# Kernel optimization log

Measured on AMD Instinct MI355X. Metric: run time of the kernel, lower is better.

## Reference

```python
import jax, jax.numpy as jnp
import numpy as np

D = 1024
H = 16
DH = D // H
F = 4096
EPS = 1e-5

def layernorm(x, gamma, beta):
    mean = jnp.mean(x, axis=-1, keepdims=True)
    var = jnp.mean((x - mean) ** 2, axis=-1, keepdims=True)  # biased variance
    return gamma * (x - mean) / jnp.sqrt(var + EPS) + beta

def setup_inputs() -> dict:
    key = jax.random.key(0)
    ks = jax.random.split(key, 12)
    s = 1.0 / np.sqrt(D)
    sf = 1.0 / np.sqrt(F)
    return {
        "x": jax.random.normal(ks[0], (16, 512, D), dtype=jnp.float32),
        "Wq": jax.random.normal(ks[1], (H, D, DH), dtype=jnp.float32) * s,
        "Wk": jax.random.normal(ks[2], (H, D, DH), dtype=jnp.float32) * s,
        "Wv": jax.random.normal(ks[3], (H, D, DH), dtype=jnp.float32) * s,
        "Wo": jax.random.normal(ks[4], (D, D), dtype=jnp.float32) * s,
        "bo": jax.random.normal(ks[5], (D,), dtype=jnp.float32) * s,
        "gamma1": jnp.ones((D,), dtype=jnp.float32),
        "beta1": jnp.zeros((D,), dtype=jnp.float32),
        "gamma2": jnp.ones((D,), dtype=jnp.float32),
        "beta2": jnp.zeros((D,), dtype=jnp.float32),
        "W1": jax.random.normal(ks[6], (D, F), dtype=jnp.float32) * s,
        "b1": jax.random.normal(ks[7], (F,), dtype=jnp.float32) * s,
        "W2": jax.random.normal(ks[8], (F, D), dtype=jnp.float32) * sf,
        "b2": jax.random.normal(ks[9], (D,), dtype=jnp.float32) * sf,
    }

def reference(x, Wq, Wk, Wv, Wo, bo, gamma1, beta1, gamma2, beta2, W1, b1, W2, b2):
    B, S, _ = x.shape
    n1 = layernorm(x, gamma1, beta1)
    # per-head projections (no bias) -> [B,H,S,DH]
    Q = jnp.einsum('bsd,hde->bhse', n1, Wq)
    K = jnp.einsum('bsd,hde->bhse', n1, Wk)
    V = jnp.einsum('bsd,hde->bhse', n1, Wv)
    scores = jnp.einsum('bhse,bhte->bhst', Q, K) / jnp.sqrt(jnp.float32(DH))
    causal = jnp.tril(jnp.ones((S, S), dtype=bool))  # keep lower triangle
    scores = jnp.where(causal, scores, -jnp.inf)
    attn = jax.nn.softmax(scores, axis=-1)  # dropout is identity at eval
    heads = jnp.einsum('bhst,bhte->bhse', attn, V)
    concat = heads.transpose(0, 2, 1, 3).reshape(B, S, D)  # concat heads in order
    x = x + (concat @ Wo + bo)
    n2 = layernorm(x, gamma2, beta2)
    ff = jax.nn.gelu(n2 @ W1 + b1, approximate=False) @ W2 + b2
    return x + ff
```

## Files before the change

### kernel.cpp

```cpp
#include <hip/hip_runtime.h>
#include <hip/hip_bf16.h>
#include <math.h>

constexpr int Dm = 1024;
constexpr int Hh = 16;
constexpr int Ff = 4096;
constexpr int Ss = 512;
constexpr int Bbatch = 16;
constexpr int NT = Bbatch * Ss;
constexpr float EPSc = 1e-5f;

typedef __attribute__((ext_vector_type(8))) short bfrag;
typedef __attribute__((ext_vector_type(4))) float f32x4;

static __device__ __forceinline__ float gelu_f(float v) {
    const float u = v * (0.7978845608f + 0.0356774081f * v * v);
    const float e = __expf(2.0f * u);
    const float th = 1.0f - 2.0f / (e + 1.0f);
    return 0.5f * v * (1.0f + th);
}

static __device__ __forceinline__ void gload16(const void* g, void* l) {
    __builtin_amdgcn_global_load_lds((__attribute__((address_space(1))) void*)g,
                                     (__attribute__((address_space(3))) void*)l,
                                     16, 0, 0);
}

#define SWZ(row, colb) ((row) * 128 + ((colb) ^ (((row) & 7) << 4)))

__global__ void __launch_bounds__(256) transpose_cvt(const float* __restrict__ in,
                                                     __hip_bfloat16* __restrict__ out,
                                                     int R, int C,
                                                     long in_zs, long out_zs) {
    __shared__ float tile[32][33];
    const float* inz = in + (size_t)blockIdx.z * in_zs;
    __hip_bfloat16* outz = out + (size_t)blockIdx.z * out_zs;
    const int c0 = blockIdx.x * 32, r0 = blockIdx.y * 32;
    const int tx = threadIdx.x & 31, ty4 = (threadIdx.x >> 5) * 4;
    #pragma unroll
    for (int i = 0; i < 4; i++)
        tile[ty4 + i][tx] = inz[(size_t)(r0 + ty4 + i) * C + c0 + tx];
    __syncthreads();
    #pragma unroll
    for (int i = 0; i < 4; i++)
        outz[(size_t)(c0 + ty4 + i) * R + r0 + tx] = __float2bfloat16(tile[tx][ty4 + i]);
}

__global__ void __launch_bounds__(256) ln_bf16(const float* __restrict__ x,
                                               const float* __restrict__ gamma,
                                               const float* __restrict__ beta,
                                               __hip_bfloat16* __restrict__ out) {
    const int row = blockIdx.x;
    const int tid = threadIdx.x;
    const int lane = tid & 63, w = tid >> 6;
    float4 xv = reinterpret_cast<const float4*>(x + (size_t)row * Dm)[tid];
    float s  = xv.x + xv.y + xv.z + xv.w;
    float ss = xv.x * xv.x + xv.y * xv.y + xv.z * xv.z + xv.w * xv.w;
    #pragma unroll
    for (int o = 32; o > 0; o >>= 1) {
        s  += __shfl_down(s,  o, 64);
        ss += __shfl_down(ss, o, 64);
    }
    __shared__ float red[2][4];
    if (lane == 0) { red[0][w] = s; red[1][w] = ss; }
    __syncthreads();
    float st  = red[0][0] + red[0][1] + red[0][2] + red[0][3];
    float sst = red[1][0] + red[1][1] + red[1][2] + red[1][3];
    float mean = st * (1.0f / Dm);
    float var  = sst * (1.0f / Dm) - mean * mean;
    float inv  = rsqrtf(var + EPSc);
    float4 g = reinterpret_cast<const float4*>(gamma)[tid];
    float4 b = reinterpret_cast<const float4*>(beta)[tid];
    __hip_bfloat16 t[4] __attribute__((aligned(8)));
    t[0] = __float2bfloat16((xv.x - mean) * inv * g.x + b.x);
    t[1] = __float2bfloat16((xv.y - mean) * inv * g.y + b.y);
    t[2] = __float2bfloat16((xv.z - mean) * inv * g.z + b.z);
    t[3] = __float2bfloat16((xv.w - mean) * inv * g.w + b.w);
    *reinterpret_cast<ushort4*>(out + (size_t)row * Dm + tid * 4) =
        *reinterpret_cast<ushort4*>(t);
}

template<int EPI>
__global__ void __launch_bounds__(256) gemm_m97(const __hip_bfloat16* __restrict__ A, int lda,
                                                const __hip_bfloat16* __restrict__ Bt, int ldb,
                                                const float* __restrict__ bias,
                                                const float* __restrict__ res,
                                                void* __restrict__ Cout, int ldc,
                                                int nbx, int K) {
    __shared__ __hip_bfloat16 As[128 * 64];
    __shared__ __hip_bfloat16 Bs[128 * 64];
    const int tid = threadIdx.x, l = tid & 63, w = tid >> 6;
    const int lr = l & 15, lg = l >> 4;
    const int nwg = gridDim.x;
    const int sbid = (blockIdx.x & 7) * (nwg >> 3) + (blockIdx.x >> 3);
    const int bx = sbid % nbx, by = sbid / nbx;
    const int m0 = by * 128, n0 = bx * 128;
    const int wr = w >> 1, wc = w & 1;
    const int srow = l >> 3;
    const int scol = ((l & 7) ^ srow) * 8;

    f32x4 acc[4][4] = {};
    for (int k0 = 0; k0 < K; k0 += 64) {
        #pragma unroll
        for (int j = 0; j < 4; j++) {
            const int rb = w * 32 + j * 8;
            gload16(A  + (size_t)(m0 + rb + srow) * lda + k0 + scol, As + rb * 64);
            gload16(Bt + (size_t)(n0 + rb + srow) * ldb + k0 + scol, Bs + rb * 64);
        }
        __syncthreads();
        #pragma unroll
        for (int kk = 0; kk < 2; kk++) {
            bfrag a[4], b[4];
            #pragma unroll
            for (int mi = 0; mi < 4; mi++) {
                const int row = wr * 64 + mi * 16 + lr;
                a[mi] = *(const bfrag*)((const char*)As + SWZ(row, (kk * 4 + lg) * 16));
            }
            #pragma unroll
            for (int ni = 0; ni < 4; ni++) {
                const int row = wc * 64 + ni * 16 + lr;
                b[ni] = *(const bfrag*)((const char*)Bs + SWZ(row, (kk * 4 + lg) * 16));
            }
            #pragma unroll
            for (int mi = 0; mi < 4; mi++)
                #pragma unroll
                for (int ni = 0; ni < 4; ni++)
                    acc[mi][ni] = __builtin_amdgcn_mfma_f32_16x16x32_bf16(a[mi], b[ni], acc[mi][ni], 0, 0, 0);
        }
        __syncthreads();
    }
    const int rb = m0 + wr * 64 + lg * 4;
    const int cb = n0 + wc * 64 + lr;
    #pragma unroll
    for (int mi = 0; mi < 4; mi++) {
        #pragma unroll
        for (int ni = 0; ni < 4; ni++) {
            #pragma unroll
            for (int rg = 0; rg < 4; rg++) {
                const int row = rb + mi * 16 + rg;
                const int col = cb + ni * 16;
                const size_t off = (size_t)row * ldc + col;
                const float v = acc[mi][ni][rg];
                if (EPI == 0) {
                    ((__hip_bfloat16*)Cout)[off] = __float2bfloat16(v);
                } else if (EPI == 1) {
                    ((float*)Cout)[off] = v + bias[col] + res[off];
                } else if (EPI == 2) {
                    ((__hip_bfloat16*)Cout)[off] = __float2bfloat16(gelu_f(v + bias[col]));
                } else {
                    ((float*)Cout)[off] = ((float*)Cout)[off] + v + bias[col];
                }
            }
        }
    }
}

__global__ void __launch_bounds__(256) attn_mfma(const __hip_bfloat16* __restrict__ QKV,
                                                 __hip_bfloat16* __restrict__ Oc) {
    constexpr int LDQ = 3072;
    __shared__ __hip_bfloat16 Qs[64 * 64];
    __shared__ __hip_bfloat16 Ks[64 * 64];
    __shared__ __hip_bfloat16 Vts[64 * 64];
    __shared__ __hip_bfloat16 Ps[4][16 * 64];
    const int tid = threadIdx.x, l = tid & 63, w = tid >> 6;
    const int lr = l & 15, lg = l >> 4;
    const int qt = blockIdx.x & 7;
    const int h  = (blockIdx.x >> 3) & 15;
    const int b  = blockIdx.x >> 7;

    const __hip_bfloat16* Qg = QKV + (size_t)(b * Ss + qt * 64) * LDQ + h * 64;
    const __hip_bfloat16* Kg = QKV + (size_t)(b * Ss) * LDQ + 1024 + h * 64;
    const __hip_bfloat16* Vg = QKV + (size_t)(b * Ss) * LDQ + 2048 + h * 64;

    const int r8 = l >> 3;
    const int scol = 8 * ((l & 7) ^ r8);

    #pragma unroll
    for (int j = 0; j < 2; j++) {
        const int slot = w * 2 + j;
        gload16(Qg + (size_t)(slot * 8 + r8) * LDQ + scol, Qs + slot * 512);
    }

    float m_run[4] = {-1e30f, -1e30f, -1e30f, -1e30f};
    float l_run[4] = {0.f, 0.f, 0.f, 0.f};
    f32x4 acc_o[4] = {};

    for (int kt = 0; kt <= qt; ++kt) {
        __syncthreads();
        #pragma unroll
        for (int j = 0; j < 2; j++) {
            const int slot = w * 2 + j;
            gload16(Kg + (size_t)(kt * 64 + slot * 8 + r8) * LDQ + scol, Ks + slot * 512);
        }
        unsigned short* vt = reinterpret_cast<unsigned short*>(Vts);
        #pragma unroll
        for (int j = 0; j < 2; j++) {
            const int e = tid + j * 256;
            const int key = e >> 3, f0 = (e & 7) * 8;
            const uint4 raw = *reinterpret_cast<const uint4*>(
                Vg + (size_t)(kt * 64 + key) * LDQ + f0);
            const unsigned int rw[4] = {raw.x, raw.y, raw.z, raw.w};
            #pragma unroll
            for (int e2 = 0; e2 < 8; e2++) {
                const int feat = f0 + e2;
                const int ad = feat * 128 + ((key * 2) ^ ((feat & 7) << 4));
                vt[ad >> 1] = (unsigned short)(rw[e2 >> 1] >> ((e2 & 1) * 16));
            }
        }
        __syncthreads();

        f32x4 s4[4] = {};
        #pragma unroll
        for (int kk = 0; kk < 2; kk++) {
            const bfrag aq = *reinterpret_cast<const bfrag*>(
                (const char*)Qs + SWZ(w * 16 + lr, kk * 64 + lg * 16));
            #pragma unroll
            for (int ni = 0; ni < 4; ni++) {
                const bfrag bk = *reinterpret_cast<const bfrag*>(
                    (const char*)Ks + SWZ(ni * 16 + lr, kk * 64 + lg * 16));
                s4[ni] = __builtin_amdgcn_mfma_f32_16x16x32_bf16(aq, bk, s4[ni], 0, 0, 0);
            }
        }
        float p[4][4];
        #pragma unroll
        for (int ni = 0; ni < 4; ni++)
            #pragma unroll
            for (int rg = 0; rg < 4; rg++)
                p[ni][rg] = s4[ni][rg] * 0.125f;
        if (kt == qt) {
            #pragma unroll
            for (int ni = 0; ni < 4; ni++)
                #pragma unroll
                for (int rg = 0; rg < 4; rg++)
                    if (ni * 16 + lr > w * 16 + lg * 4 + rg) p[ni][rg] = -1e30f;
        }
        float sf[4];
        #pragma unroll
        for (int rg = 0; rg < 4; rg++) {
            float mx = fmaxf(fmaxf(p[0][rg], p[1][rg]), fmaxf(p[2][rg], p[3][rg]));
            #pragma unroll
            for (int o = 1; o < 16; o <<= 1) mx = fmaxf(mx, __shfl_xor(mx, o, 64));
            const float mn = fmaxf(m_run[rg], mx);
            sf[rg] = __expf(m_run[rg] - mn);
            m_run[rg] = mn;
        }
        float rsum[4] = {};
        #pragma unroll
        for (int ni = 0; ni < 4; ni++)
            #pragma unroll
            for (int rg = 0; rg < 4; rg++) {
                const float e = __expf(p[ni][rg] - m_run[rg]);
                p[ni][rg] = e;
                rsum[rg] += e;
            }
        #pragma unroll
        for (int rg = 0; rg < 4; rg++) {
            #pragma unroll
            for (int o = 1; o < 16; o <<= 1) rsum[rg] += __shfl_xor(rsum[rg], o, 64);
            l_run[rg] = l_run[rg] * sf[rg] + rsum[rg];
        }
        #pragma unroll
        for (int di = 0; di < 4; di++)
            #pragma unroll
            for (int rg = 0; rg < 4; rg++)
                acc_o[di][rg] *= sf[rg];
        unsigned short* pw = reinterpret_cast<unsigned short*>(Ps[w]);
        #pragma unroll
        for (int ni = 0; ni < 4; ni++)
            #pragma unroll
            for (int rg = 0; rg < 4; rg++) {
                const int prow = lg * 4 + rg;
                const int ad = SWZ(prow, (ni * 16 + lr) * 2);
                __hip_bfloat16 pb = __float2bfloat16(p[ni][rg]);
                pw[ad >> 1] = *reinterpret_cast<unsigned short*>(&pb);
            }
        #pragma unroll
        for (int kk = 0; kk < 2; kk++) {
            const bfrag pa = *reinterpret_cast<const bfrag*>(
                (const char*)Ps[w] + SWZ(lr, kk * 64 + lg * 16));
            #pragma unroll
            for (int di = 0; di < 4; di++) {
                const bfrag vb = *reinterpret_cast<const bfrag*>(
                    (const char*)Vts + SWZ(di * 16 + lr, kk * 64 + lg * 16));
                acc_o[di] = __builtin_amdgcn_mfma_f32_16x16x32_bf16(pa, vb, acc_o[di], 0, 0, 0);
            }
        }
    }
    #pragma unroll
    for (int di = 0; di < 4; di++)
        #pragma unroll
        for (int rg = 0; rg < 4; rg++) {
            const int q = qt * 64 + w * 16 + lg * 4 + rg;
            const float v = acc_o[di][rg] / l_run[rg];
            Oc[(size_t)(b * Ss + q) * Dm + h * 64 + di * 16 + lr] = __float2bfloat16(v);
        }
}

extern "C" void kernel_launch(void* const* d_in, const int* in_sizes, int n_in,
                              void* d_out, int out_size, void* d_ws, size_t ws_size,
                              hipStream_t stream) {
    const float* x   = (const float*)d_in[0];
    const float* Wq  = (const float*)d_in[1];
    const float* Wk  = (const float*)d_in[2];
    const float* Wv  = (const float*)d_in[3];
    const float* Wo  = (const float*)d_in[4];
    const float* bo  = (const float*)d_in[5];
    const float* g1  = (const float*)d_in[6];
    const float* be1 = (const float*)d_in[7];
    const float* g2  = (const float*)d_in[8];
    const float* be2 = (const float*)d_in[9];
    const float* W1  = (const float*)d_in[10];
    const float* b1  = (const float*)d_in[11];
    const float* W2  = (const float*)d_in[12];
    const float* b2  = (const float*)d_in[13];
    float* out = (float*)d_out;

    char* wsb = (char*)d_ws;
    __hip_bfloat16* WqkvT = (__hip_bfloat16*)(wsb);
    __hip_bfloat16* WoT   = (__hip_bfloat16*)(wsb + 6291456);
    __hip_bfloat16* W1T   = (__hip_bfloat16*)(wsb + 8388608);
    __hip_bfloat16* W2T   = (__hip_bfloat16*)(wsb + 16777216);
    __hip_bfloat16* n1    = (__hip_bfloat16*)(wsb + 25165824);
    __hip_bfloat16* QKV   = (__hip_bfloat16*)(wsb + 41943040);
    __hip_bfloat16* concat = n1;
    __hip_bfloat16* n2     = n1;
    __hip_bfloat16* h1     = QKV;

    transpose_cvt<<<dim3(2, 32, 16), 256, 0, stream>>>(Wq, WqkvT,              1024, 64, 65536, 65536);
    transpose_cvt<<<dim3(2, 32, 16), 256, 0, stream>>>(Wk, WqkvT + 1024 * 1024, 1024, 64, 65536, 65536);
    transpose_cvt<<<dim3(2, 32, 16), 256, 0, stream>>>(Wv, WqkvT + 2048 * 1024, 1024, 64, 65536, 65536);
    transpose_cvt<<<dim3(32, 32, 1), 256, 0, stream>>>(Wo, WoT, 1024, 1024, 0, 0);
    transpose_cvt<<<dim3(128, 32, 1), 256, 0, stream>>>(W1, W1T, 1024, 4096, 0, 0);
    transpose_cvt<<<dim3(32, 128, 1), 256, 0, stream>>>(W2, W2T, 4096, 1024, 0, 0);

    ln_bf16<<<NT, 256, 0, stream>>>(x, g1, be1, n1);
    gemm_m97<0><<<1536, 256, 0, stream>>>(n1, Dm, WqkvT, Dm, nullptr, nullptr,
                                          QKV, 3072, 24, Dm);
    attn_mfma<<<NT * Hh / 64, 256, 0, stream>>>(QKV, concat);
    gemm_m97<1><<<512, 256, 0, stream>>>(concat, Dm, WoT, Dm, bo, x,
                                         out, Dm, 8, Dm);
    ln_bf16<<<NT, 256, 0, stream>>>(out, g2, be2, n2);
    gemm_m97<2><<<2048, 256, 0, stream>>>(n2, Dm, W1T, Dm, b1, nullptr,
                                          h1, Ff, 32, Dm);
    gemm_m97<3><<<512, 256, 0, stream>>>(h1, Ff, W2T, Ff, b2, nullptr,
                                         out, Dm, 8, Ff);
}
```

Baseline: 425.8 us.

## Double-buffer GEMM LDS tiles to overlap global loads with MFMA compute

Converts the bf16 MFMA GEMM to a two-stage LDS ping-pong. The next K tile is issued with direct-to-LDS loads while the current tile is consumed, and a partial vmcnt wait replaces the full-drain __syncthreads. It also raises wave priority around the MFMA block. LDS use per block doubles to 64 KB, which may reduce occupancy.

Result: faster. 402.6 us (-5.4%).

```diff
diff --git a/kernel.cpp b/kernel.cpp
--- a/kernel.cpp
+++ b/kernel.cpp
@@ -81,14 +81,14 @@
 }
 
 template<int EPI>
-__global__ void __launch_bounds__(256) gemm_m97(const __hip_bfloat16* __restrict__ A, int lda,
-                                                const __hip_bfloat16* __restrict__ Bt, int ldb,
-                                                const float* __restrict__ bias,
-                                                const float* __restrict__ res,
-                                                void* __restrict__ Cout, int ldc,
-                                                int nbx, int K) {
-    __shared__ __hip_bfloat16 As[128 * 64];
-    __shared__ __hip_bfloat16 Bs[128 * 64];
+__global__ void __launch_bounds__(256) gemm_db(const __hip_bfloat16* __restrict__ A, int lda,
+                                               const __hip_bfloat16* __restrict__ Bt, int ldb,
+                                               const float* __restrict__ bias,
+                                               const float* __restrict__ res,
+                                               void* __restrict__ Cout, int ldc,
+                                               int nbx, int K) {
+    __shared__ __hip_bfloat16 As[2][128 * 64];
+    __shared__ __hip_bfloat16 Bs[2][128 * 64];
     const int tid = threadIdx.x, l = tid & 63, w = tid >> 6;
     const int lr = l & 15, lg = l >> 4;
     const int nwg = gridDim.x;
@@ -98,36 +98,55 @@
     const int wr = w >> 1, wc = w & 1;
     const int srow = l >> 3;
     const int scol = ((l & 7) ^ srow) * 8;
-
-    f32x4 acc[4][4] = {};
-    for (int k0 = 0; k0 < K; k0 += 64) {
+    const int NK = K >> 6;
+
+    auto STAGE = [&](int t, int bsel) {
+        const int k0 = t * 64;
         #pragma unroll
         for (int j = 0; j < 4; j++) {
             const int rb = w * 32 + j * 8;
-            gload16(A  + (size_t)(m0 + rb + srow) * lda + k0 + scol, As + rb * 64);
-            gload16(Bt + (size_t)(n0 + rb + srow) * ldb + k0 + scol, Bs + rb * 64);
-        }
-        __syncthreads();
+            gload16(A  + (size_t)(m0 + rb + srow) * lda + k0 + scol, &As[bsel][rb * 64]);
+            gload16(Bt + (size_t)(n0 + rb + srow) * ldb + k0 + scol, &Bs[bsel][rb * 64]);
+        }
+    };
+
+    f32x4 acc[4][4] = {};
+    STAGE(0, 0);
+    for (int t = 0; t < NK; t++) {
+        const int cur = t & 1;
+        if (t + 1 < NK) {
+            STAGE(t + 1, cur ^ 1);
+            asm volatile("s_waitcnt vmcnt(8)" ::: "memory");
+        } else {
+            asm volatile("s_waitcnt vmcnt(0)" ::: "memory");
+        }
+        __builtin_amdgcn_s_barrier();
+        __builtin_amdgcn_sched_barrier(0);
+        const char* Ab = (const char*)&As[cur][0];
+        const char* Bb = (const char*)&Bs[cur][0];
         #pragma unroll
         for (int kk = 0; kk < 2; kk++) {
             bfrag a[4], b[4];
             #pragma unroll
             for (int mi = 0; mi < 4; mi++) {
                 const int row = wr * 64 + mi * 16 + lr;
-                a[mi] = *(const bfrag*)((const char*)As + SWZ(row, (kk * 4 + lg) * 16));
+                a[mi] = *(const bfrag*)(Ab + SWZ(row, (kk * 4 + lg) * 16));
             }
             #pragma unroll
             for (int ni = 0; ni < 4; ni++) {
                 const int row = wc * 64 + ni * 16 + lr;
-                b[ni] = *(const bfrag*)((const char*)Bs + SWZ(row, (kk * 4 + lg) * 16));
-            }
+                b[ni] = *(const bfrag*)(Bb + SWZ(row, (kk * 4 + lg) * 16));
+            }
+            __builtin_amdgcn_s_setprio(1);
             #pragma unroll
             for (int mi = 0; mi < 4; mi++)
                 #pragma unroll
                 for (int ni = 0; ni < 4; ni++)
                     acc[mi][ni] = __builtin_amdgcn_mfma_f32_16x16x32_bf16(a[mi], b[ni], acc[mi][ni], 0, 0, 0);
-        }
-        __syncthreads();
+            __builtin_amdgcn_s_setprio(0);
+        }
+        __builtin_amdgcn_sched_barrier(0);
+        __builtin_amdgcn_s_barrier();
     }
     const int rb = m0 + wr * 64 + lg * 4;
     const int cb = n0 + wc * 64 + lr;
@@ -334,14 +353,14 @@
     transpose_cvt<<<dim3(32, 128, 1), 256, 0, stream>>>(W2, W2T, 4096, 1024, 0, 0);
 
     ln_bf16<<<NT, 256, 0, stream>>>(x, g1, be1, n1);
-    gemm_m97<0><<<1536, 256, 0, stream>>>(n1, Dm, WqkvT, Dm, nullptr, nullptr,
-                                          QKV, 3072, 24, Dm);
+    gemm_db<0><<<1536, 256, 0, stream>>>(n1, Dm, WqkvT, Dm, nullptr, nullptr,
+                                         QKV, 3072, 24, Dm);
     attn_mfma<<<NT * Hh / 64, 256, 0, stream>>>(QKV, concat);
-    gemm_m97<1><<<512, 256, 0, stream>>>(concat, Dm, WoT, Dm, bo, x,
-                                         out, Dm, 8, Dm);
+    gemm_db<1><<<512, 256, 0, stream>>>(concat, Dm, WoT, Dm, bo, x,
+                                        out, Dm, 8, Dm);
     ln_bf16<<<NT, 256, 0, stream>>>(out, g2, be2, n2);
-    gemm_m97<2><<<2048, 256, 0, stream>>>(n2, Dm, W1T, Dm, b1, nullptr,
-                                          h1, Ff, 32, Dm);
-    gemm_m97<3><<<512, 256, 0, stream>>>(h1, Ff, W2T, Ff, b2, nullptr,
-                                         out, Dm, 8, Ff);
-}
+    gemm_db<2><<<2048, 256, 0, stream>>>(n2, Dm, W1T, Dm, b1, nullptr,
+                                         h1, Ff, 32, Dm);
+    gemm_db<3><<<512, 256, 0, stream>>>(h1, Ff, W2T, Ff, b2, nullptr,
+                                        out, Dm, 8, Ff);
+}
```
